# Optimization experiments

Hardware: AMD Instinct MI355X
Metric: run time of the kernel (lower is better)

## Reference

```python
import jax, jax.numpy as jnp
import numpy as np

TWO_N, D = 8192, 256
N = TWO_N // 2


def setup_inputs() -> dict:
    key = jax.random.key(0)
    k1, k2 = jax.random.split(key)
    embeddings = jax.random.normal(k1, (TWO_N, D), dtype=jnp.float32)
    pos_mask = jnp.zeros((N, TWO_N), dtype=bool)  # unused by the loss
    neg_mask = jax.random.randint(k2, (N, TWO_N), 0, 2).astype(bool)
    return {"embeddings": embeddings, "pos_mask": pos_mask, "neg_mask": neg_mask}


def reference(embeddings, pos_mask, neg_mask):
    # d[i, j] = <e_i, e_j>  (other_embeddings defaults to embeddings)
    d = jnp.matmul(embeddings, embeddings.T)            # [2N, 2N]
    n = embeddings.shape[0] // 2
    rows = d[:n]                                        # [N, 2N] (only rows 0..N-1 used)
    ap = rows[jnp.arange(n), jnp.arange(n) + n]         # d[i, i+N], shape [N]
    # masked sum_j exp(d[i,j] - ap_i) over negatives, then log(1 + .)
    expm = jnp.exp(rows - ap[:, None])                  # [N, 2N]
    j_all = jnp.log1p(jnp.sum(jnp.where(neg_mask, expm, 0.0), axis=1))  # [N]
    return jnp.mean(j_all)
```

## Files before the change

### kernel.cpp

```cpp
#include <hip/hip_runtime.h>
#include <math.h>

#define TWO_N 8192
#define NR 4096
#define D 256
#define PMW 128
#define L2E 1.44269504088896340736f

typedef __attribute__((ext_vector_type(8))) short bf16x8;
typedef __attribute__((ext_vector_type(4))) float f32x4;

#define AS1V const __attribute__((address_space(1))) void
#define AS3V __attribute__((address_space(3))) void
#define WAITVM(n) asm volatile("s_waitcnt vmcnt(" #n ")" ::: "memory")

__device__ inline unsigned short f2bf(float x) {
  unsigned u = __builtin_bit_cast(unsigned, x);
  u += 0x7fffu + ((u >> 16) & 1u);
  return (unsigned short)(u >> 16);
}

__device__ inline float exp2_hw(float x) {
  float r;
  asm("v_exp_f32 %0, %1" : "=v"(r) : "v"(x));
  return r;
}

__global__ __launch_bounds__(256) void prep_kernel(
    const float* __restrict__ emb, const unsigned char* __restrict__ negm,
    unsigned short* __restrict__ ebf, unsigned long long* __restrict__ pm,
    float* __restrict__ apl, double* __restrict__ rowsum) {
  const int b = blockIdx.x, t = threadIdx.x;
  if (b < 1024) {
    const size_t i = ((size_t)b * 256 + t) * 8;
    const float4 a = *reinterpret_cast<const float4*>(emb + i);
    const float4 c = *reinterpret_cast<const float4*>(emb + i + 4);
    union { unsigned short s[8]; bf16x8 v; } o;
    o.s[0] = f2bf(a.x); o.s[1] = f2bf(a.y); o.s[2] = f2bf(a.z); o.s[3] = f2bf(a.w);
    o.s[4] = f2bf(c.x); o.s[5] = f2bf(c.y); o.s[6] = f2bf(c.z); o.s[7] = f2bf(c.w);
    *reinterpret_cast<bf16x8*>(ebf + i) = o.v;
  } else if (b < 3072) {
    const int w = (b - 1024) * 256 + t;
    const uint4* p = reinterpret_cast<const uint4*>(negm + (size_t)w * 64);
    unsigned long long acc = 0;
#pragma unroll
    for (int q = 0; q < 4; ++q) {
      const uint4 v = p[q];
      unsigned bb = 0;
      bb |= (v.x & 1u) | ((v.x >> 7) & 2u) | ((v.x >> 14) & 4u) | ((v.x >> 21) & 8u);
      bb |= ((v.y & 1u) | ((v.y >> 7) & 2u) | ((v.y >> 14) & 4u) | ((v.y >> 21) & 8u)) << 4;
      bb |= ((v.z & 1u) | ((v.z >> 7) & 2u) | ((v.z >> 14) & 4u) | ((v.z >> 21) & 8u)) << 8;
      bb |= ((v.w & 1u) | ((v.w >> 7) & 2u) | ((v.w >> 14) & 4u) | ((v.w >> 21) & 8u)) << 12;
      acc |= (unsigned long long)bb << (q * 16);
    }
    pm[w] = acc;
  } else {
    const int lane = t & 63, wid = t >> 6;
    const int i = (b - 3072) * 4 + wid;
    const float4 a = *reinterpret_cast<const float4*>(emb + (size_t)i * D + lane * 4);
    const float4 c = *reinterpret_cast<const float4*>(emb + (size_t)(i + NR) * D + lane * 4);
    float s = a.x * c.x + a.y * c.y + a.z * c.z + a.w * c.w;
#pragma unroll
    for (int off = 32; off >= 1; off >>= 1) s += __shfl_xor(s, off, 64);
    if (lane == 0) { apl[i] = -s * L2E; rowsum[i] = 0.0; }
  }
}

__global__ __launch_bounds__(512) void fused_mfma(
    const unsigned short* __restrict__ ebf, const unsigned long long* __restrict__ pm,
    const float* __restrict__ apl, double* __restrict__ rowsum) {
  __shared__ unsigned short As[4][128 * 64];
  __shared__ unsigned short Bs[2][256 * 64];
  const int t = threadIdx.x, lane = t & 63, wid = t >> 6;
  const int wr = wid >> 2, wc = wid & 3;
  const int bi = blockIdx.x >> 3;
  const int chunk = blockIdx.x & 7;
  const int g = lane >> 4, cl = lane & 15;
  const int srow = lane >> 3;
  const int sc8 = ((lane & 7) ^ srow) * 8;

  float apv[4][4];
#pragma unroll
  for (int m = 0; m < 4; ++m) {
    const float4 v = *reinterpret_cast<const float4*>(apl + bi * 128 + wr * 64 + m * 16 + g * 4);
    apv[m][0] = v.x; apv[m][1] = v.y; apv[m][2] = v.z; apv[m][3] = v.w;
  }

#pragma unroll
  for (int kt = 0; kt < 4; ++kt)
#pragma unroll
    for (int q = 0; q < 2; ++q) {
      const int rbase = wid * 16 + q * 8;
      const unsigned short* gp = ebf + (size_t)(bi * 128 + rbase + srow) * D + kt * 64 + sc8;
      __builtin_amdgcn_global_load_lds((AS1V*)gp, (AS3V*)(As[kt] + rbase * 64), 16, 0, 0);
    }

  auto STAGEB = [&](int gk) {
    const int kt = gk & 3, bjj = gk >> 2;
#pragma unroll
    for (int q = 0; q < 4; ++q) {
      const int rbase = wid * 32 + q * 8;
      const unsigned short* gp =
          ebf + (size_t)(chunk * 1024 + bjj * 256 + rbase + srow) * D + kt * 64 + sc8;
      __builtin_amdgcn_global_load_lds((AS1V*)gp, (AS3V*)(Bs[gk & 1] + rbase * 64), 16, 0, 0);
    }
  };
  STAGEB(0); STAGEB(1);

  double rs[4][4] = {};

  for (int bj = 0; bj < 4; ++bj) {
    f32x4 acc[4][4] = {};
    unsigned long long mw[4][4];
#pragma unroll
    for (int kt = 0; kt < 4; ++kt) {
      const int gkt = bj * 4 + kt;
      if (kt == 3) { if (bj == 3) { WAITVM(0); } else { WAITVM(4); } }
      else { WAITVM(4); }
      __builtin_amdgcn_s_barrier();
      __builtin_amdgcn_sched_barrier(0);
      __builtin_amdgcn_s_setprio(1);
#pragma unroll
      for (int kk = 0; kk < 2; ++kk) {
        const int cswz = ((kk * 4 + g) ^ (lane & 7)) * 8;
        bf16x8 af[4], bf[4];
#pragma unroll
        for (int m = 0; m < 4; ++m)
          af[m] = *reinterpret_cast<const bf16x8*>(&As[kt][(wr * 64 + m * 16 + cl) * 64 + cswz]);
#pragma unroll
        for (int n = 0; n < 4; ++n)
          bf[n] = *reinterpret_cast<const bf16x8*>(&Bs[gkt & 1][(wc * 64 + n * 16 + cl) * 64 + cswz]);
#pragma unroll
        for (int m = 0; m < 4; ++m)
#pragma unroll
          for (int n = 0; n < 4; ++n)
            acc[m][n] = __builtin_amdgcn_mfma_f32_16x16x32_bf16(af[m], bf[n], acc[m][n], 0, 0, 0);
      }
      __builtin_amdgcn_s_setprio(0);
      __builtin_amdgcn_s_barrier();
      __builtin_amdgcn_sched_barrier(0);
      if (kt == 3) {
#pragma unroll
        for (int m = 0; m < 4; ++m)
#pragma unroll
          for (int r2 = 0; r2 < 4; ++r2) {
            const int row = bi * 128 + wr * 64 + m * 16 + g * 4 + r2;
            mw[m][r2] = pm[(size_t)row * PMW + chunk * 16 + bj * 4 + wc];
          }
        __builtin_amdgcn_sched_barrier(0);
      }
      if (gkt + 2 < 16) STAGEB(gkt + 2);
      __builtin_amdgcn_sched_barrier(0);
    }
#pragma unroll
    for (int m = 0; m < 4; ++m)
#pragma unroll
      for (int n = 0; n < 4; ++n)
#pragma unroll
        for (int r2 = 0; r2 < 4; ++r2) {
          float tt = fmaf(acc[m][n][r2], L2E, apv[m][r2]);
          tt = fminf(fmaxf(tt, -1020.f), 1000.f);
          const float kf = floorf(tt);
          const float mant = exp2_hw(tt - kf);
          const float mm = ((mw[m][r2] >> (n * 16 + cl)) & 1) ? mant : 0.f;
          const long long ebits = (long long)(1023 + (int)kf) << 52;
          rs[m][r2] += (double)mm * __builtin_bit_cast(double, ebits);
        }
  }

#pragma unroll
  for (int m = 0; m < 4; ++m)
#pragma unroll
    for (int r2 = 0; r2 < 4; ++r2) {
      double v = rs[m][r2];
#pragma unroll
      for (int off = 8; off >= 1; off >>= 1) v += __shfl_xor(v, off, 64);
      if (cl == 0) atomicAdd(&rowsum[bi * 128 + wr * 64 + m * 16 + g * 4 + r2], v);
    }
}

__global__ __launch_bounds__(1024) void finalize_kernel(const double* __restrict__ rowsum,
                                                        float* __restrict__ out) {
  __shared__ double red[16];
  const int t = threadIdx.x;
  double s = 0.0;
#pragma unroll
  for (int k = 0; k < 4; ++k) s += log1p(rowsum[t + k * 1024]);
#pragma unroll
  for (int off = 32; off >= 1; off >>= 1) s += __shfl_xor(s, off, 64);
  if ((t & 63) == 0) red[t >> 6] = s;
  __syncthreads();
  if (t == 0) {
    double tot = 0.0;
#pragma unroll
    for (int w = 0; w < 16; ++w) tot += red[w];
    out[0] = (float)(tot * (1.0 / NR));
  }
}

extern "C" void kernel_launch(void* const* d_in, const int* in_sizes, int n_in,
                              void* d_out, int out_size, void* d_ws, size_t ws_size,
                              hipStream_t stream) {
  const float* emb = (const float*)d_in[0];
  const unsigned char* negm = (const unsigned char*)d_in[2];
  float* out = (float*)d_out;
  char* ws = (char*)d_ws;
  unsigned short* ebf = (unsigned short*)ws;
  unsigned long long* pm = (unsigned long long*)(ws + (1u << 22));
  float* apl = (float*)(ws + (2u << 22));
  double* rowsum = (double*)(ws + (2u << 22) + 16384);

  prep_kernel<<<dim3(4096), dim3(256), 0, stream>>>(emb, negm, ebf, pm, apl, rowsum);
  fused_mfma<<<dim3(256), dim3(512), 0, stream>>>(ebf, pm, apl, rowsum);
  finalize_kernel<<<dim3(1), dim3(1024), 0, stream>>>(rowsum, out);
}
```

Measured before the change: 265.4 us.

## Shrink GEMM tile to 128x128 with 256 threads and two blocks per CU

The fused MFMA kernel changes from 512-thread blocks computing 128x256 tiles (whole A strip resident in LDS) to 256-thread blocks computing 128x128 tiles. A and B are now double-buffered together per k-step, which cuts LDS use to 64KB so two blocks can share a CU. The grid doubles to 512 blocks, with the column range split into halves per XCD-mapped chunk. The aim is more occupancy and better latency hiding, at the cost of re-streaming A tiles each bj iteration and lower reuse of B per block.

```diff
diff --git a/kernel.cpp b/kernel.cpp
--- a/kernel.cpp
+++ b/kernel.cpp
@@ -66,15 +66,18 @@
   }
 }
 
-__global__ __launch_bounds__(512) void fused_mfma(
+__global__ __launch_bounds__(256, 2) void fused_mfma(
     const unsigned short* __restrict__ ebf, const unsigned long long* __restrict__ pm,
     const float* __restrict__ apl, double* __restrict__ rowsum) {
-  __shared__ unsigned short As[4][128 * 64];
-  __shared__ unsigned short Bs[2][256 * 64];
+  __shared__ unsigned short As[2][128 * 64];
+  __shared__ unsigned short Bs[2][128 * 64];
   const int t = threadIdx.x, lane = t & 63, wid = t >> 6;
-  const int wr = wid >> 2, wc = wid & 3;
-  const int bi = blockIdx.x >> 3;
-  const int chunk = blockIdx.x & 7;
+  const int wr = wid >> 1, wc = wid & 1;
+  const int xcd = blockIdx.x & 7;
+  const int idx = blockIdx.x >> 3;
+  const int bi = idx >> 1;
+  const int half = idx & 1;
+  const int colbase = xcd * 1024 + half * 512;
   const int g = lane >> 4, cl = lane & 15;
   const int srow = lane >> 3;
   const int sc8 = ((lane & 7) ^ srow) * 8;
@@ -86,37 +89,30 @@
     apv[m][0] = v.x; apv[m][1] = v.y; apv[m][2] = v.z; apv[m][3] = v.w;
   }
 
-#pragma unroll
-  for (int kt = 0; kt < 4; ++kt)
-#pragma unroll
-    for (int q = 0; q < 2; ++q) {
-      const int rbase = wid * 16 + q * 8;
-      const unsigned short* gp = ebf + (size_t)(bi * 128 + rbase + srow) * D + kt * 64 + sc8;
-      __builtin_amdgcn_global_load_lds((AS1V*)gp, (AS3V*)(As[kt] + rbase * 64), 16, 0, 0);
-    }
-
-  auto STAGEB = [&](int gk) {
-    const int kt = gk & 3, bjj = gk >> 2;
+  auto STAGE = [&](int s) {
+    const int kt = s & 3, bj = s >> 2, slot = s & 1;
 #pragma unroll
     for (int q = 0; q < 4; ++q) {
       const int rbase = wid * 32 + q * 8;
-      const unsigned short* gp =
-          ebf + (size_t)(chunk * 1024 + bjj * 256 + rbase + srow) * D + kt * 64 + sc8;
-      __builtin_amdgcn_global_load_lds((AS1V*)gp, (AS3V*)(Bs[gk & 1] + rbase * 64), 16, 0, 0);
+      const unsigned short* gA = ebf + (size_t)(bi * 128 + rbase + srow) * D + kt * 64 + sc8;
+      const unsigned short* gB =
+          ebf + (size_t)(colbase + bj * 128 + rbase + srow) * D + kt * 64 + sc8;
+      __builtin_amdgcn_global_load_lds((AS1V*)gA, (AS3V*)(As[slot] + rbase * 64), 16, 0, 0);
+      __builtin_amdgcn_global_load_lds((AS1V*)gB, (AS3V*)(Bs[slot] + rbase * 64), 16, 0, 0);
     }
   };
-  STAGEB(0); STAGEB(1);
+  STAGE(0); STAGE(1);
 
   double rs[4][4] = {};
 
+#pragma unroll
   for (int bj = 0; bj < 4; ++bj) {
     f32x4 acc[4][4] = {};
     unsigned long long mw[4][4];
 #pragma unroll
     for (int kt = 0; kt < 4; ++kt) {
-      const int gkt = bj * 4 + kt;
-      if (kt == 3) { if (bj == 3) { WAITVM(0); } else { WAITVM(4); } }
-      else { WAITVM(4); }
+      const int s = bj * 4 + kt, slot = kt & 1;
+      if (bj == 3 && kt == 3) { WAITVM(0); } else { WAITVM(8); }
       __builtin_amdgcn_s_barrier();
       __builtin_amdgcn_sched_barrier(0);
       __builtin_amdgcn_s_setprio(1);
@@ -126,10 +122,10 @@
         bf16x8 af[4], bf[4];
 #pragma unroll
         for (int m = 0; m < 4; ++m)
-          af[m] = *reinterpret_cast<const bf16x8*>(&As[kt][(wr * 64 + m * 16 + cl) * 64 + cswz]);
+          af[m] = *reinterpret_cast<const bf16x8*>(&As[slot][(wr * 64 + m * 16 + cl) * 64 + cswz]);
 #pragma unroll
         for (int n = 0; n < 4; ++n)
-          bf[n] = *reinterpret_cast<const bf16x8*>(&Bs[gkt & 1][(wc * 64 + n * 16 + cl) * 64 + cswz]);
+          bf[n] = *reinterpret_cast<const bf16x8*>(&Bs[slot][(wc * 64 + n * 16 + cl) * 64 + cswz]);
 #pragma unroll
         for (int m = 0; m < 4; ++m)
 #pragma unroll
@@ -145,11 +141,11 @@
 #pragma unroll
           for (int r2 = 0; r2 < 4; ++r2) {
             const int row = bi * 128 + wr * 64 + m * 16 + g * 4 + r2;
-            mw[m][r2] = pm[(size_t)row * PMW + chunk * 16 + bj * 4 + wc];
+            mw[m][r2] = pm[(size_t)row * PMW + xcd * 16 + half * 8 + bj * 2 + wc];
           }
         __builtin_amdgcn_sched_barrier(0);
       }
-      if (gkt + 2 < 16) STAGEB(gkt + 2);
+      if (s + 2 < 16) STAGE(s + 2);
       __builtin_amdgcn_sched_barrier(0);
     }
 #pragma unroll
@@ -211,6 +207,6 @@
   double* rowsum = (double*)(ws + (2u << 22) + 16384);
 
   prep_kernel<<<dim3(4096), dim3(256), 0, stream>>>(emb, negm, ebf, pm, apl, rowsum);
-  fused_mfma<<<dim3(256), dim3(512), 0, stream>>>(ebf, pm, apl, rowsum);
+  fused_mfma<<<dim3(512), dim3(256), 0, stream>>>(ebf, pm, apl, rowsum);
   finalize_kernel<<<dim3(1), dim3(1024), 0, stream>>>(rowsum, out);
 }
```

New measurement: 373.9 us. +40.9%, slower.
